# Performance work log

Measured on AMD Instinct MI355X. Metric: run time of the kernel, lower is better.

The kernel has to match this reference:

```python
import jax, jax.numpy as jnp
import numpy as np

ROWS, COLS, N_CHARS = 384, 768, 69  # CHARSET length = 69
CH, CW = 28, 14  # char tile height, width


def setup_inputs() -> dict:
    key = jax.random.key(0)
    k1, k2 = jax.random.split(key)
    grid_logits = jax.random.normal(k1, (ROWS, COLS, N_CHARS), dtype=jnp.float32)
    # font rasterizations are in [0, 1] (pixel intensity / 255)
    font = jax.random.uniform(k2, (N_CHARS, CH, CW), dtype=jnp.float32)
    return {"grid_logits": grid_logits, "font": font}


def reference(grid_logits, font):
    rows, cols, n_chars = grid_logits.shape
    ch, cw = font.shape[1], font.shape[2]
    # softmax over characters per grid cell
    probs = jax.nn.softmax(grid_logits, axis=-1)  # (R, C, N)
    # soft blend of font tiles: (R, C, ch, cw)
    soft_tiles = jnp.einsum('rcn,nhw->rchw', probs, font)
    # assemble full image: equivalent to nested torch.cat over rows/cols
    soft_image = soft_tiles.transpose(0, 2, 1, 3).reshape(rows * ch, cols * cw)
    return soft_image[None, None]  # (1, 1, H, W)
```

## Files before the change

kernel.cpp:

```cpp
#include <hip/hip_runtime.h>
#include <hip/hip_bf16.h>

#define ROWS 384
#define COLS 768
#define NCH  69
#define CH   28
#define CW   14
#define KP   96
#define IMG_W 10752
#define ROW_U 72
#define CHUNK_B (64 * NCH * 4)

typedef __attribute__((ext_vector_type(8))) short bfrag;
typedef __attribute__((ext_vector_type(4))) float f32x4;

__device__ __forceinline__ unsigned bf16bits(float x) {
    unsigned b = __float_as_uint(x);
    b += 0x7FFFu + ((b >> 16) & 1u);
    return b >> 16;
}

__device__ __forceinline__ void gload_lds16(const void* g, void* l) {
    __builtin_amdgcn_global_load_lds(
        (const __attribute__((address_space(1))) void*)g,
        (__attribute__((address_space(3))) void*)l, 16, 0, 0);
}

__global__ __launch_bounds__(256)
void font_prep(const float* __restrict__ font, unsigned short* __restrict__ Fh) {
    int idx = blockIdx.x * 256 + threadIdx.x;
    if (idx >= CH * 16 * KP) return;
    int k  = idx % KP;
    int hw = idx / KP;
    int w  = hw % 16, h = hw / 16;
    float v = (w < CW && k < NCH) ? font[k * (CH * CW) + h * CW + w] : 0.f;
    Fh[idx] = (unsigned short)bf16bits(v);
}

__global__ __launch_bounds__(128, 2)
void diffrender_v15(const float* __restrict__ logits,
                    const unsigned short* __restrict__ Fh,
                    float* __restrict__ out)
{
    __shared__ __align__(16) unsigned char smem[2][CHUNK_B];

    const int tid  = threadIdx.x;
    const int lane = tid & 63;
    const int wv   = tid >> 6;
    const int r    = blockIdx.x / 6;
    const int cb   = (blockIdx.x % 6) * 128;

    unsigned char* wch = smem[wv];

    const char* gbase = (const char*)logits
                      + (size_t)(blockIdx.x * 128 + wv * 64) * (NCH * 4);
#pragma unroll
    for (int i = 0; i < 18; ++i) {
        const int off = (i < 17) ? i * 1024 : (CHUNK_B - 1024);
        gload_lds16(gbase + off + lane * 16, (void*)(wch + off));
    }
    asm volatile("s_waitcnt vmcnt(0)" ::: "memory");

    const float* myrow = (const float*)(wch + (size_t)lane * (NCH * 4));
    float e[NCH];
    float m = -INFINITY;
#pragma unroll
    for (int n = 0; n < NCH; ++n) { e[n] = myrow[n]; m = fmaxf(m, e[n]); }
    float s = 0.f;
#pragma unroll
    for (int n = 0; n < NCH; ++n) { e[n] = __expf(e[n] - m); s += e[n]; }
    const float inv = 1.f / s;

    unsigned* prow = (unsigned*)(wch + (size_t)lane * (ROW_U * 2));
#pragma unroll
    for (int i = 0; i < 34; ++i)
        prow[i] = bf16bits(e[2 * i] * inv) | (bf16bits(e[2 * i + 1] * inv) << 16);
    prow[34] = bf16bits(e[68] * inv);
    prow[35] = 0;

    const int w15   = lane & 15;
    const int g     = lane >> 4;
    const int kgrp  = g * 8;
    const int crow4 = g * 4;
    const unsigned short* pa = (const unsigned short*)wch;
    bfrag a[4][3];
#pragma unroll
    for (int mt = 0; mt < 4; ++mt) {
        const size_t base = (size_t)(mt * 16 + w15) * ROW_U;
        a[mt][0] = *(const bfrag*)&pa[base + kgrp];
        a[mt][1] = *(const bfrag*)&pa[base + 32 + kgrp];
        a[mt][2] = *(const bfrag*)&pa[base + 64];
    }

    float* stage = (float*)wch;

    const unsigned short* fb = Fh + (size_t)w15 * KP + kgrp;
    bfrag bcur[2][3], bnxt[2][3];
#pragma unroll
    for (int hh = 0; hh < 2; ++hh)
#pragma unroll
        for (int ks = 0; ks < 3; ++ks)
            bcur[hh][ks] = *(const bfrag*)(fb + (size_t)(hh * 16) * KP + ks * 32);

#pragma unroll 1
    for (int h2 = 0; h2 < CH / 2; ++h2) {
        const int h = 2 * h2;
        if (h2 + 1 < CH / 2) {
            const unsigned short* fn = fb + (size_t)((h + 2) * 16) * KP;
#pragma unroll
            for (int hh = 0; hh < 2; ++hh)
#pragma unroll
                for (int ks = 0; ks < 3; ++ks)
                    bnxt[hh][ks] = *(const bfrag*)(fn + (size_t)(hh * 16) * KP + ks * 32);
        }

        f32x4 acc[2][4];
#pragma unroll
        for (int hh = 0; hh < 2; ++hh)
#pragma unroll
            for (int mt = 0; mt < 4; ++mt)
                acc[hh][mt] = f32x4{0, 0, 0, 0};
#pragma unroll
        for (int hh = 0; hh < 2; ++hh)
#pragma unroll
            for (int mt = 0; mt < 4; ++mt)
#pragma unroll
                for (int ks = 0; ks < 3; ++ks)
                    acc[hh][mt] = __builtin_amdgcn_mfma_f32_16x16x32_bf16(
                        a[mt][ks], bcur[hh][ks], acc[hh][mt], 0, 0, 0);

        if (w15 < CW) {
#pragma unroll
            for (int hh = 0; hh < 2; ++hh)
#pragma unroll
                for (int mt = 0; mt < 4; ++mt)
#pragma unroll
                    for (int j = 0; j < 4; ++j)
                        stage[hh * 896 + (mt * 16 + crow4 + j) * CW + w15] = acc[hh][mt][j];
        }

#pragma unroll
        for (int hh = 0; hh < 2; ++hh) {
            f32x4* o4 = (f32x4*)(out + (size_t)(r * CH + h + hh) * IMG_W
                                     + (size_t)(cb + wv * 64) * CW);
            const f32x4* s4 = (const f32x4*)(stage + hh * 896);
#pragma unroll
            for (int i = 0; i < 4; ++i) {
                const int idx = i * 64 + lane;
                if (idx < 224) __builtin_nontemporal_store(s4[idx], &o4[idx]);
            }
        }

#pragma unroll
        for (int hh = 0; hh < 2; ++hh)
#pragma unroll
            for (int ks = 0; ks < 3; ++ks)
                bcur[hh][ks] = bnxt[hh][ks];
    }
}

extern "C" void kernel_launch(void* const* d_in, const int* in_sizes, int n_in,
                              void* d_out, int out_size, void* d_ws, size_t ws_size,
                              hipStream_t stream) {
    const float* logits = (const float*)d_in[0];
    const float* font   = (const float*)d_in[1];
    float* out          = (float*)d_out;
    unsigned short* Fh  = (unsigned short*)d_ws;

    font_prep<<<(CH * 16 * KP + 255) / 256, 256, 0, stream>>>(font, Fh);

    const int blocks = (ROWS * COLS) / 128;
    diffrender_v15<<<blocks, 128, 0, stream>>>(logits, Fh, out);
}
```

Baseline: 106.6 us.

## Make render kernel persistent with double-buffered prefetch of next logits chunk

New measurement: 108.3 us. Within noise of the previous version (+1.6%).

```diff
diff --git a/kernel.cpp b/kernel.cpp
--- a/kernel.cpp
+++ b/kernel.cpp
@@ -10,6 +10,10 @@
 #define IMG_W 10752
 #define ROW_U 72
 #define CHUNK_B (64 * NCH * 4)
+#define PROB_B  (64 * ROW_U * 2)
+#define NCHUNKS (ROWS * COLS / 128)
+#define BLOCKS_P 768
+#define CPB 3
 
 typedef __attribute__((ext_vector_type(8))) short bfrag;
 typedef __attribute__((ext_vector_type(4))) float f32x4;
@@ -37,125 +41,148 @@
     Fh[idx] = (unsigned short)bf16bits(v);
 }
 
-__global__ __launch_bounds__(128, 2)
-void diffrender_v15(const float* __restrict__ logits,
+__global__ __launch_bounds__(128)
+void diffrender_v16(const float* __restrict__ logits,
                     const unsigned short* __restrict__ Fh,
                     float* __restrict__ out)
 {
-    __shared__ __align__(16) unsigned char smem[2][CHUNK_B];
+    __shared__ __align__(16) unsigned char bufA[2][CHUNK_B];
+    __shared__ __align__(16) unsigned char bufB[2][PROB_B];
 
     const int tid  = threadIdx.x;
     const int lane = tid & 63;
     const int wv   = tid >> 6;
-    const int r    = blockIdx.x / 6;
-    const int cb   = (blockIdx.x % 6) * 128;
-
-    unsigned char* wch = smem[wv];
-
-    const char* gbase = (const char*)logits
-                      + (size_t)(blockIdx.x * 128 + wv * 64) * (NCH * 4);
-#pragma unroll
-    for (int i = 0; i < 18; ++i) {
-        const int off = (i < 17) ? i * 1024 : (CHUNK_B - 1024);
-        gload_lds16(gbase + off + lane * 16, (void*)(wch + off));
-    }
-    asm volatile("s_waitcnt vmcnt(0)" ::: "memory");
-
-    const float* myrow = (const float*)(wch + (size_t)lane * (NCH * 4));
-    float e[NCH];
-    float m = -INFINITY;
-#pragma unroll
-    for (int n = 0; n < NCH; ++n) { e[n] = myrow[n]; m = fmaxf(m, e[n]); }
-    float s = 0.f;
-#pragma unroll
-    for (int n = 0; n < NCH; ++n) { e[n] = __expf(e[n] - m); s += e[n]; }
-    const float inv = 1.f / s;
-
-    unsigned* prow = (unsigned*)(wch + (size_t)lane * (ROW_U * 2));
-#pragma unroll
-    for (int i = 0; i < 34; ++i)
-        prow[i] = bf16bits(e[2 * i] * inv) | (bf16bits(e[2 * i + 1] * inv) << 16);
-    prow[34] = bf16bits(e[68] * inv);
-    prow[35] = 0;
+    unsigned char* A = bufA[wv];
+    unsigned char* B = bufB[wv];
 
     const int w15   = lane & 15;
     const int g     = lane >> 4;
     const int kgrp  = g * 8;
     const int crow4 = g * 4;
-    const unsigned short* pa = (const unsigned short*)wch;
-    bfrag a[4][3];
-#pragma unroll
-    for (int mt = 0; mt < 4; ++mt) {
-        const size_t base = (size_t)(mt * 16 + w15) * ROW_U;
-        a[mt][0] = *(const bfrag*)&pa[base + kgrp];
-        a[mt][1] = *(const bfrag*)&pa[base + 32 + kgrp];
-        a[mt][2] = *(const bfrag*)&pa[base + 64];
+    const unsigned short* fb = Fh + (size_t)w15 * KP + kgrp;
+
+    int cid = blockIdx.x;
+
+    {
+        const char* gb = (const char*)logits + (size_t)(cid * 128 + wv * 64) * (NCH * 4);
+#pragma unroll
+        for (int i = 0; i < 18; ++i) {
+            const int off = (i < 17) ? i * 1024 : (CHUNK_B - 1024);
+            gload_lds16(gb + off + lane * 16, (void*)(A + off));
+        }
     }
 
-    float* stage = (float*)wch;
-
-    const unsigned short* fb = Fh + (size_t)w15 * KP + kgrp;
-    bfrag bcur[2][3], bnxt[2][3];
-#pragma unroll
-    for (int hh = 0; hh < 2; ++hh)
-#pragma unroll
-        for (int ks = 0; ks < 3; ++ks)
-            bcur[hh][ks] = *(const bfrag*)(fb + (size_t)(hh * 16) * KP + ks * 32);
-
 #pragma unroll 1
-    for (int h2 = 0; h2 < CH / 2; ++h2) {
-        const int h = 2 * h2;
-        if (h2 + 1 < CH / 2) {
-            const unsigned short* fn = fb + (size_t)((h + 2) * 16) * KP;
+    for (int c = 0; c < CPB; ++c) {
+        asm volatile("s_waitcnt vmcnt(0)" ::: "memory");
+
+        const int r  = cid / 6;
+        const int cb = (cid % 6) * 128;
+
+        const float* myrow = (const float*)(A + (size_t)lane * (NCH * 4));
+        float e[NCH];
+        float m = -INFINITY;
+#pragma unroll
+        for (int n = 0; n < NCH; ++n) { e[n] = myrow[n]; m = fmaxf(m, e[n]); }
+        float s = 0.f;
+#pragma unroll
+        for (int n = 0; n < NCH; ++n) { e[n] = __expf(e[n] - m); s += e[n]; }
+        const float inv = 1.f / s;
+
+        if (c + 1 < CPB) {
+            asm volatile("s_waitcnt lgkmcnt(0)" ::: "memory");
+            const char* gb = (const char*)logits
+                           + (size_t)((cid + BLOCKS_P) * 128 + wv * 64) * (NCH * 4);
+#pragma unroll
+            for (int i = 0; i < 18; ++i) {
+                const int off = (i < 17) ? i * 1024 : (CHUNK_B - 1024);
+                gload_lds16(gb + off + lane * 16, (void*)(A + off));
+            }
+        }
+
+        unsigned* prow = (unsigned*)(B + (size_t)lane * (ROW_U * 2));
+#pragma unroll
+        for (int i = 0; i < 34; ++i)
+            prow[i] = bf16bits(e[2 * i] * inv) | (bf16bits(e[2 * i + 1] * inv) << 16);
+        prow[34] = bf16bits(e[68] * inv);
+        prow[35] = 0;
+
+        const unsigned short* pa = (const unsigned short*)B;
+        bfrag a[4][3];
+#pragma unroll
+        for (int mt = 0; mt < 4; ++mt) {
+            const size_t base = (size_t)(mt * 16 + w15) * ROW_U;
+            a[mt][0] = *(const bfrag*)&pa[base + kgrp];
+            a[mt][1] = *(const bfrag*)&pa[base + 32 + kgrp];
+            a[mt][2] = *(const bfrag*)&pa[base + 64];
+        }
+
+        float* stage = (float*)B;
+
+        bfrag bcur[2][3], bnxt[2][3];
+#pragma unroll
+        for (int hh = 0; hh < 2; ++hh)
+#pragma unroll
+            for (int ks = 0; ks < 3; ++ks)
+                bcur[hh][ks] = *(const bfrag*)(fb + (size_t)(hh * 16) * KP + ks * 32);
+
+#pragma unroll 1
+        for (int h2 = 0; h2 < CH / 2; ++h2) {
+            const int h = 2 * h2;
+            if (h2 + 1 < CH / 2) {
+                const unsigned short* fn = fb + (size_t)((h + 2) * 16) * KP;
+#pragma unroll
+                for (int hh = 0; hh < 2; ++hh)
+#pragma unroll
+                    for (int ks = 0; ks < 3; ++ks)
+                        bnxt[hh][ks] = *(const bfrag*)(fn + (size_t)(hh * 16) * KP + ks * 32);
+            }
+
+            f32x4 acc[2][4];
 #pragma unroll
             for (int hh = 0; hh < 2; ++hh)
 #pragma unroll
+                for (int mt = 0; mt < 4; ++mt)
+                    acc[hh][mt] = f32x4{0, 0, 0, 0};
+#pragma unroll
+            for (int hh = 0; hh < 2; ++hh)
+#pragma unroll
+                for (int mt = 0; mt < 4; ++mt)
+#pragma unroll
+                    for (int ks = 0; ks < 3; ++ks)
+                        acc[hh][mt] = __builtin_amdgcn_mfma_f32_16x16x32_bf16(
+                            a[mt][ks], bcur[hh][ks], acc[hh][mt], 0, 0, 0);
+
+            if (w15 < CW) {
+#pragma unroll
+                for (int hh = 0; hh < 2; ++hh)
+#pragma unroll
+                    for (int mt = 0; mt < 4; ++mt)
+#pragma unroll
+                        for (int j = 0; j < 4; ++j)
+                            stage[hh * 896 + (mt * 16 + crow4 + j) * CW + w15] = acc[hh][mt][j];
+            }
+
+#pragma unroll
+            for (int hh = 0; hh < 2; ++hh) {
+                f32x4* o4 = (f32x4*)(out + (size_t)(r * CH + h + hh) * IMG_W
+                                         + (size_t)(cb + wv * 64) * CW);
+                const f32x4* s4 = (const f32x4*)(stage + hh * 896);
+#pragma unroll
+                for (int i = 0; i < 4; ++i) {
+                    const int idx = i * 64 + lane;
+                    if (idx < 224) __builtin_nontemporal_store(s4[idx], &o4[idx]);
+                }
+            }
+
+#pragma unroll
+            for (int hh = 0; hh < 2; ++hh)
+#pragma unroll
                 for (int ks = 0; ks < 3; ++ks)
-                    bnxt[hh][ks] = *(const bfrag*)(fn + (size_t)(hh * 16) * KP + ks * 32);
-        }
-
-        f32x4 acc[2][4];
-#pragma unroll
-        for (int hh = 0; hh < 2; ++hh)
-#pragma unroll
-            for (int mt = 0; mt < 4; ++mt)
-                acc[hh][mt] = f32x4{0, 0, 0, 0};
-#pragma unroll
-        for (int hh = 0; hh < 2; ++hh)
-#pragma unroll
-            for (int mt = 0; mt < 4; ++mt)
-#pragma unroll
-                for (int ks = 0; ks < 3; ++ks)
-                    acc[hh][mt] = __builtin_amdgcn_mfma_f32_16x16x32_bf16(
-                        a[mt][ks], bcur[hh][ks], acc[hh][mt], 0, 0, 0);
-
-        if (w15 < CW) {
-#pragma unroll
-            for (int hh = 0; hh < 2; ++hh)
-#pragma unroll
-                for (int mt = 0; mt < 4; ++mt)
-#pragma unroll
-                    for (int j = 0; j < 4; ++j)
-                        stage[hh * 896 + (mt * 16 + crow4 + j) * CW + w15] = acc[hh][mt][j];
-        }
-
-#pragma unroll
-        for (int hh = 0; hh < 2; ++hh) {
-            f32x4* o4 = (f32x4*)(out + (size_t)(r * CH + h + hh) * IMG_W
-                                     + (size_t)(cb + wv * 64) * CW);
-            const f32x4* s4 = (const f32x4*)(stage + hh * 896);
-#pragma unroll
-            for (int i = 0; i < 4; ++i) {
-                const int idx = i * 64 + lane;
-                if (idx < 224) __builtin_nontemporal_store(s4[idx], &o4[idx]);
-            }
-        }
-
-#pragma unroll
-        for (int hh = 0; hh < 2; ++hh)
-#pragma unroll
-            for (int ks = 0; ks < 3; ++ks)
-                bcur[hh][ks] = bnxt[hh][ks];
+                    bcur[hh][ks] = bnxt[hh][ks];
+        }
+
+        cid += BLOCKS_P;
     }
 }
 
@@ -169,6 +196,5 @@
 
     font_prep<<<(CH * 16 * KP + 255) / 256, 256, 0, stream>>>(font, Fh);
 
-    const int blocks = (ROWS * COLS) / 128;
-    diffrender_v15<<<blocks, 128, 0, stream>>>(logits, Fh, out);
-}
+    diffrender_v16<<<BLOCKS_P, 128, 0, stream>>>(logits, Fh, out);
+}
```
